# Kernel tuning notes

Hardware: AMD Instinct MI355X
Metric: run time of the kernel (lower is better)

Reference implementation:

```python
import jax, jax.numpy as jnp
import numpy as np

N = 20000       # nodes
E = 320000      # edges (before self-loops)
F_IN = 1024     # num_features
H = 4           # head_num
C = 64          # hidden_size
NC = 4          # n_classes
NEG_SLOPE = 0.2 # PyG GATConv default


def setup_inputs() -> dict:
    key = jax.random.key(0)
    ks = jax.random.split(key, 16)
    def w(k, shape, fan_in):
        return jax.random.normal(k, shape, dtype=jnp.float32) / np.sqrt(fan_in)
    x = jax.random.normal(ks[0], (N, F_IN), dtype=jnp.float32)
    edge_index = jax.random.randint(ks[1], (2, E), 0, N, dtype=jnp.int64)
    return {
        "x": x,
        "edge_index": edge_index,
        # layer 1: F_IN -> H*C, concat
        "w1": w(ks[2], (F_IN, H * C), F_IN),
        "as1": w(ks[3], (H, C), C),
        "ad1": w(ks[4], (H, C), C),
        "b1": jnp.zeros((H * C,), jnp.float32),
        # layer 2: H*C -> H*C, concat
        "w2": w(ks[5], (H * C, H * C), H * C),
        "as2": w(ks[6], (H, C), C),
        "ad2": w(ks[7], (H, C), C),
        "b2": jnp.zeros((H * C,), jnp.float32),
        # out layer: H*C -> C, 1 head, concat=False
        "w3": w(ks[8], (H * C, 1 * C), H * C),
        "as3": w(ks[9], (1, C), C),
        "ad3": w(ks[10], (1, C), C),
        "b3": jnp.zeros((C,), jnp.float32),
        # classifier
        "wc": w(ks[11], (C, NC), C),
        "bc": jnp.zeros((NC,), jnp.float32),
    }


def gat_layer(x, src, dst, W, a_src, a_dst, bias, concat):
    """PyG GATConv (eval mode, self-loops already added to src/dst)."""
    n = x.shape[0]
    Hh, Cc = a_src.shape
    h = (x @ W).reshape(n, Hh, Cc)                       # [N,H,C]
    al_s = jnp.sum(h * a_src[None], axis=-1)             # [N,H]
    al_d = jnp.sum(h * a_dst[None], axis=-1)             # [N,H]
    e = al_s[src] + al_d[dst]                            # [E,H]
    e = jax.nn.leaky_relu(e, NEG_SLOPE)
    # segment softmax over incoming edges of each destination node
    emax = jax.ops.segment_max(e, dst, num_segments=n)   # [N,H]
    ex = jnp.exp(e - emax[dst])
    denom = jax.ops.segment_sum(ex, dst, num_segments=n) # [N,H]
    alpha = ex / (denom[dst] + 1e-16)                    # [E,H]
    msg = h[src] * alpha[..., None]                      # [E,H,C]
    out = jax.ops.segment_sum(msg, dst, num_segments=n)  # [N,H,C]
    if concat:
        out = out.reshape(n, Hh * Cc)
    else:
        out = out.mean(axis=1)
    return out + bias


def reference(x, edge_index, w1, as1, ad1, b1, w2, as2, ad2, b2,
              w3, as3, ad3, b3, wc, bc):
    n = x.shape[0]
    loop = jnp.arange(n, dtype=edge_index.dtype)
    src = jnp.concatenate([edge_index[0], loop])
    dst = jnp.concatenate([edge_index[1], loop])
    out = jax.nn.relu(gat_layer(x, src, dst, w1, as1, ad1, b1, True))
    out = jax.nn.relu(gat_layer(out, src, dst, w2, as2, ad2, b2, True))
    out = gat_layer(out, src, dst, w3, as3, ad3, b3, False)
    return out @ wc + bc                                  # [N, n_classes]
```

## Files before the change

kernel.cpp:

```cpp
#include <hip/hip_runtime.h>

#define N_NODES 20000
#define N_EDGES 320000
#define ET (N_EDGES + N_NODES)
#define F_IN 1024
#define HC 256
#define NC 4

typedef unsigned short ushort_t;
typedef __attribute__((ext_vector_type(8))) short short8;
typedef __attribute__((ext_vector_type(4))) float f32x4;

__device__ inline ushort_t f2bf(float f) {
    unsigned u = __float_as_uint(f);
    unsigned r = (u + 0x7fffu + ((u >> 16) & 1u)) >> 16;
    return (ushort_t)r;
}
__device__ inline float bf2f(ushort_t u) {
    return __uint_as_float(((unsigned)u) << 16);
}

#define GLOAD16(gp, lp) __builtin_amdgcn_global_load_lds( \
    (const __attribute__((address_space(1))) void*)(gp),  \
    (__attribute__((address_space(3))) void*)(lp), 16, 0, 0)

__global__ void count_kernel(const int* __restrict__ ei, int* __restrict__ counts) {
    int e = blockIdx.x * blockDim.x + threadIdx.x;
    if (e >= ET) return;
    int dst = (e < N_EDGES) ? ei[N_EDGES + e] : (e - N_EDGES);
    atomicAdd(&counts[dst], 1);
}

__global__ void scan_kernel(const int* __restrict__ counts, int* __restrict__ row_ptr,
                            int* __restrict__ cursor) {
    __shared__ int sums[1024];
    int t = threadIdx.x;
    const int per = (N_NODES + 1023) / 1024;
    int b = t * per;
    int e = min(b + per, N_NODES);
    int s = 0;
    for (int i = b; i < e; ++i) s += counts[i];
    sums[t] = s;
    __syncthreads();
    for (int off = 1; off < 1024; off <<= 1) {
        int v = (t >= off) ? sums[t - off] : 0;
        __syncthreads();
        sums[t] += v;
        __syncthreads();
    }
    int run = (t == 0) ? 0 : sums[t - 1];
    for (int i = b; i < e; ++i) {
        row_ptr[i] = run;
        cursor[i]  = run;
        run += counts[i];
    }
    if (t == 0) row_ptr[N_NODES] = ET;
}

__global__ void scatter_kernel(const int* __restrict__ ei, int* __restrict__ cursor,
                               int* __restrict__ col) {
    int e = blockIdx.x * blockDim.x + threadIdx.x;
    if (e >= ET) return;
    int src, dst;
    if (e < N_EDGES) { src = ei[e]; dst = ei[N_EDGES + e]; }
    else             { src = dst = e - N_EDGES; }
    int pos = atomicAdd(&cursor[dst], 1);
    col[pos] = src;
}

__global__ void split_rows(const float* __restrict__ in, ushort_t* __restrict__ hi,
                           ushort_t* __restrict__ lo, int n4) {
    int i = blockIdx.x * blockDim.x + threadIdx.x;
    int stride = gridDim.x * blockDim.x;
    for (; i < n4; i += stride) {
        float4 v = ((const float4*)in)[i];
        ushort4 h, l;
        h.x = f2bf(v.x); l.x = f2bf(v.x - bf2f(h.x));
        h.y = f2bf(v.y); l.y = f2bf(v.y - bf2f(h.y));
        h.z = f2bf(v.z); l.z = f2bf(v.z - bf2f(h.z));
        h.w = f2bf(v.w); l.w = f2bf(v.w - bf2f(h.w));
        ((ushort4*)hi)[i] = h;
        ((ushort4*)lo)[i] = l;
    }
}

__global__ void split_T(const float* __restrict__ in, ushort_t* __restrict__ hi,
                        ushort_t* __restrict__ lo, int K, int Nn) {
    int idx = blockIdx.x * blockDim.x + threadIdx.x;
    if (idx >= K * Nn) return;
    int k = idx / Nn, n = idx - k * Nn;
    float v = in[idx];
    ushort_t h = f2bf(v);
    hi[(size_t)n * K + k] = h;
    lo[(size_t)n * K + k] = f2bf(v - bf2f(h));
}

template<int BM, int BN, int GY>
__launch_bounds__(256)
__global__ void gemm_mfma(const ushort_t* __restrict__ Ah, const ushort_t* __restrict__ Al,
                          const ushort_t* __restrict__ BTh, const ushort_t* __restrict__ BTl,
                          float* __restrict__ C, int M, int K, int NT) {
    constexpr int SM = BM / 2;
    constexpr int SN = BN / 2;
    constexpr int MF = SM / 16;
    constexpr int NF = SN / 16;
    constexpr int AQ = BM / 64;
    constexpr int BQ = BN / 64;
    __shared__ __align__(16) ushort_t smem[(2 * BM + 2 * BN) * 32];
    char* Ash = (char*)smem;
    char* Asl = Ash + BM * 64;
    char* Bsh = Asl + BM * 64;
    char* Bsl = Bsh + BN * 64;

    const int t = threadIdx.x, lane = t & 63, w = t >> 6;
    const int wm = w >> 1, wn = w & 1;
    const int nwg = gridDim.x;
    const int id = blockIdx.x;
    const int q = nwg >> 3, r = nwg & 7;
    const int xcd = id & 7, idx = id >> 3;
    const int logical = (xcd < r ? xcd * (q + 1) : r * (q + 1) + (xcd - r) * q) + idx;
    const int bm = (logical / GY) * BM, bn = (logical % GY) * BN;
    const int gchunk = ((lane & 3) ^ ((lane >> 3) & 3)) * 16;

    size_t gA[AQ]; int lA[AQ];
    #pragma unroll
    for (int qq = 0; qq < AQ; ++qq) {
        int inst = w * AQ + qq;
        int row  = inst * 16 + (lane >> 2);
        int grow = min(bm + row, M - 1);
        gA[qq] = (size_t)grow * K * 2 + gchunk;
        lA[qq] = inst * 1024;
    }
    size_t gB[BQ]; int lB[BQ];
    #pragma unroll
    for (int qq = 0; qq < BQ; ++qq) {
        int inst = w * BQ + qq;
        int row  = inst * 16 + (lane >> 2);
        gB[qq] = (size_t)(bn + row) * K * 2 + gchunk;
        lB[qq] = inst * 1024;
    }

    f32x4 acc[MF][NF];
    #pragma unroll
    for (int i = 0; i < MF; ++i)
        #pragma unroll
        for (int j = 0; j < NF; ++j) acc[i][j] = (f32x4){0.f, 0.f, 0.f, 0.f};

    const char* Ahb = (const char*)Ah;
    const char* Alb = (const char*)Al;
    const char* Bhb = (const char*)BTh;
    const char* Blb = (const char*)BTl;
    const int c16 = (lane >> 4);

    for (int k0 = 0; k0 < K; k0 += 32) {
        size_t kb = (size_t)k0 * 2;
        #pragma unroll
        for (int qq = 0; qq < AQ; ++qq) {
            GLOAD16(Ahb + gA[qq] + kb, Ash + lA[qq]);
            GLOAD16(Alb + gA[qq] + kb, Asl + lA[qq]);
        }
        #pragma unroll
        for (int qq = 0; qq < BQ; ++qq) {
            GLOAD16(Bhb + gB[qq] + kb, Bsh + lB[qq]);
            GLOAD16(Blb + gB[qq] + kb, Bsl + lB[qq]);
        }
        __syncthreads();
        short8 afh[MF], afl[MF], bfh[NF], bfl[NF];
        #pragma unroll
        for (int i = 0; i < MF; ++i) {
            int row = wm * SM + i * 16 + (lane & 15);
            int off = row * 64 + ((c16 ^ ((row >> 1) & 3)) * 16);
            afh[i] = *(const short8*)(Ash + off);
            afl[i] = *(const short8*)(Asl + off);
        }
        #pragma unroll
        for (int j = 0; j < NF; ++j) {
            int row = wn * SN + j * 16 + (lane & 15);
            int off = row * 64 + ((c16 ^ ((row >> 1) & 3)) * 16);
            bfh[j] = *(const short8*)(Bsh + off);
            bfl[j] = *(const short8*)(Bsl + off);
        }
        #pragma unroll
        for (int i = 0; i < MF; ++i)
            #pragma unroll
            for (int j = 0; j < NF; ++j) {
                acc[i][j] = __builtin_amdgcn_mfma_f32_16x16x32_bf16(afh[i], bfh[j], acc[i][j], 0, 0, 0);
                acc[i][j] = __builtin_amdgcn_mfma_f32_16x16x32_bf16(afh[i], bfl[j], acc[i][j], 0, 0, 0);
                acc[i][j] = __builtin_amdgcn_mfma_f32_16x16x32_bf16(afl[i], bfh[j], acc[i][j], 0, 0, 0);
            }
        __syncthreads();
    }
    #pragma unroll
    for (int i = 0; i < MF; ++i) {
        int rbase = bm + wm * SM + i * 16 + (lane >> 4) * 4;
        #pragma unroll
        for (int j = 0; j < NF; ++j) {
            int col = bn + wn * SN + j * 16 + (lane & 15);
            #pragma unroll
            for (int rr = 0; rr < 4; ++rr)
                if (rbase + rr < M) C[(size_t)(rbase + rr) * NT + col] = acc[i][j][rr];
        }
    }
}

template<int H>
__global__ void al_kernel(const float* __restrict__ h, const float* __restrict__ as_w,
                          const float* __restrict__ ad_w, float* __restrict__ als,
                          float* __restrict__ ald) {
    int n = blockIdx.x;
    int t = threadIdx.x;
    float hv = h[(size_t)n * (H * 64) + t];
    float s = hv * as_w[t];
    float d = hv * ad_w[t];
    #pragma unroll
    for (int off = 32; off > 0; off >>= 1) {
        s += __shfl_down(s, off, 64);
        d += __shfl_down(d, off, 64);
    }
    if ((t & 63) == 0) {
        int head = t >> 6;
        als[n * H + head] = s;
        ald[n * H + head] = d;
    }
}

template<bool SPLIT>
__launch_bounds__(256)
__global__ void agg4_kernel(const float* __restrict__ h, const float* __restrict__ als,
                            const float* __restrict__ ald, const int* __restrict__ row_ptr,
                            const int* __restrict__ col, const float* __restrict__ bias,
                            ushort_t* __restrict__ oh, ushort_t* __restrict__ ol,
                            float* __restrict__ of) {
    int dst = blockIdx.x;
    int t = threadIdx.x, lane = t & 63, w = t >> 6;
    int beg = row_ptr[dst], deg = row_ptr[dst + 1] - beg;
    __shared__ float s_redm[4][4], s_redd[4][4];
    __shared__ float s_m[4], s_rden[4];
    __shared__ int   s_src[64];
    __shared__ float s_alpha[64][4];
    __shared__ float4 s_part[3][64];

    int i_loc = t >> 2, hh = t & 3;
    float ad = ald[dst * 4 + hh];

    float m = -1e30f, den = 0.f;
    for (int base = 0; base < deg; base += 64) {
        int i = base + i_loc;
        if (i < deg) {
            int src = col[beg + i];
            float e = als[src * 4 + hh] + ad;
            e = (e > 0.f) ? e : 0.2f * e;
            float nm = fmaxf(m, e);
            den = den * __expf(m - nm) + __expf(e - nm);
            m = nm;
        }
    }
    #pragma unroll
    for (int off = 4; off < 64; off <<= 1) {
        float mo = __shfl_xor(m, off, 64);
        float dn = __shfl_xor(den, off, 64);
        float nm = fmaxf(m, mo);
        den = den * __expf(m - nm) + dn * __expf(mo - nm);
        m = nm;
    }
    if (lane < 4) { s_redm[w][lane] = m; s_redd[w][lane] = den; }
    __syncthreads();
    if (t < 4) {
        float M = -1e30f, D = 0.f;
        #pragma unroll
        for (int ww = 0; ww < 4; ++ww) {
            float mo = s_redm[ww][t], dn = s_redd[ww][t];
            float nm = fmaxf(M, mo);
            D = D * __expf(M - nm) + dn * __expf(mo - nm);
            M = nm;
        }
        s_m[t] = M;
        s_rden[t] = 1.f / (D + 1e-16f);
    }
    __syncthreads();

    float mh = s_m[hh], rdh = s_rden[hh];
    float4 acc = make_float4(0.f, 0.f, 0.f, 0.f);
    int c = lane;
    int ghead = c >> 4;
    for (int base = 0; base < deg; base += 64) {
        int cn = min(64, deg - base);
        if (i_loc < cn) {
            int src = col[beg + base + i_loc];
            if (hh == 0) s_src[i_loc] = src;
            float e = als[src * 4 + hh] + ad;
            e = (e > 0.f) ? e : 0.2f * e;
            s_alpha[i_loc][hh] = __expf(e - mh) * rdh;
        }
        __syncthreads();
        for (int e = w; e < cn; e += 4) {
            int src = s_src[e];
            float a = s_alpha[e][ghead];
            float4 hv = *(const float4*)&h[(size_t)src * HC + c * 4];
            acc.x += a * hv.x; acc.y += a * hv.y;
            acc.z += a * hv.z; acc.w += a * hv.w;
        }
        __syncthreads();
    }
    if (w > 0) s_part[w - 1][c] = acc;
    __syncthreads();
    if (w == 0) {
        float4 p1 = s_part[0][c], p2 = s_part[1][c], p3 = s_part[2][c];
        float4 bv = *(const float4*)&bias[c * 4];
        float v0 = fmaxf(((acc.x + p1.x) + p2.x) + p3.x + bv.x, 0.f);
        float v1 = fmaxf(((acc.y + p1.y) + p2.y) + p3.y + bv.y, 0.f);
        float v2 = fmaxf(((acc.z + p1.z) + p2.z) + p3.z + bv.z, 0.f);
        float v3 = fmaxf(((acc.w + p1.w) + p2.w) + p3.w + bv.w, 0.f);
        size_t idx = (size_t)dst * HC + c * 4;
        if (SPLIT) {
            ushort4 h4, l4;
            h4.x = f2bf(v0); l4.x = f2bf(v0 - bf2f(h4.x));
            h4.y = f2bf(v1); l4.y = f2bf(v1 - bf2f(h4.y));
            h4.z = f2bf(v2); l4.z = f2bf(v2 - bf2f(h4.z));
            h4.w = f2bf(v3); l4.w = f2bf(v3 - bf2f(h4.w));
            *(ushort4*)&oh[idx] = h4;
            *(ushort4*)&ol[idx] = l4;
        } else {
            *(float4*)&of[idx] = make_float4(v0, v1, v2, v3);
        }
    }
}

__launch_bounds__(256)
__global__ void agg1_kernel(const float* __restrict__ h, const float* __restrict__ als,
                            const float* __restrict__ ald, const int* __restrict__ row_ptr,
                            const int* __restrict__ col, const float* __restrict__ bias,
                            float* __restrict__ of) {
    __shared__ int   s1_src[4][64];
    __shared__ float s1_alpha[4][64];
    int lane = threadIdx.x & 63, w = threadIdx.x >> 6;
    int dst = blockIdx.x * 4 + w;
    if (dst >= N_NODES) return;
    int beg = row_ptr[dst], deg = row_ptr[dst + 1] - beg;
    float ad = ald[dst];

    float m = -1e30f, den = 0.f;
    for (int base = 0; base < deg; base += 64) {
        int i = base + lane;
        if (i < deg) {
            float e = als[col[beg + i]] + ad;
            e = (e > 0.f) ? e : 0.2f * e;
            float nm = fmaxf(m, e);
            den = den * __expf(m - nm) + __expf(e - nm);
            m = nm;
        }
    }
    #pragma unroll
    for (int off = 1; off < 64; off <<= 1) {
        float mo = __shfl_xor(m, off, 64);
        float dn = __shfl_xor(den, off, 64);
        float nm = fmaxf(m, mo);
        den = den * __expf(m - nm) + dn * __expf(mo - nm);
        m = nm;
    }
    float rden = 1.f / (den + 1e-16f);

    float4 acc = make_float4(0.f, 0.f, 0.f, 0.f);
    int c = lane & 15, team = lane >> 4;
    for (int base = 0; base < deg; base += 64) {
        int cn = min(64, deg - base);
        if (lane < cn) {
            int src = col[beg + base + lane];
            s1_src[w][lane] = src;
            float e = als[src] + ad;
            e = (e > 0.f) ? e : 0.2f * e;
            s1_alpha[w][lane] = __expf(e - m) * rden;
        }
        for (int e = team; e < cn; e += 4) {
            float a = s1_alpha[w][e];
            float4 hv = *(const float4*)&h[(size_t)s1_src[w][e] * 64 + c * 4];
            acc.x += a * hv.x; acc.y += a * hv.y;
            acc.z += a * hv.z; acc.w += a * hv.w;
        }
    }
    acc.x += __shfl_xor(acc.x, 16, 64);
    acc.y += __shfl_xor(acc.y, 16, 64);
    acc.z += __shfl_xor(acc.z, 16, 64);
    acc.w += __shfl_xor(acc.w, 16, 64);
    acc.x += __shfl_xor(acc.x, 32, 64);
    acc.y += __shfl_xor(acc.y, 32, 64);
    acc.z += __shfl_xor(acc.z, 32, 64);
    acc.w += __shfl_xor(acc.w, 32, 64);
    if (team == 0) {
        float4 bv = *(const float4*)&bias[c * 4];
        *(float4*)&of[(size_t)dst * 64 + c * 4] =
            make_float4(acc.x + bv.x, acc.y + bv.y, acc.z + bv.z, acc.w + bv.w);
    }
}

__global__ void classifier_kernel(const float* __restrict__ x, const float* __restrict__ wc,
                                  const float* __restrict__ bc, float* __restrict__ out) {
    int n = blockIdx.x * blockDim.x + threadIdx.x;
    if (n >= N_NODES) return;
    float acc[NC] = {bc[0], bc[1], bc[2], bc[3]};
    for (int c = 0; c < 64; ++c) {
        float xv = x[(size_t)n * 64 + c];
        #pragma unroll
        for (int k = 0; k < NC; ++k) acc[k] += xv * wc[c * NC + k];
    }
    #pragma unroll
    for (int k = 0; k < NC; ++k) out[(size_t)n * NC + k] = acc[k];
}

extern "C" void kernel_launch(void* const* d_in, const int* in_sizes, int n_in,
                              void* d_out, int out_size, void* d_ws, size_t ws_size,
                              hipStream_t stream) {
    const float* x   = (const float*)d_in[0];
    const int*   ei  = (const int*)d_in[1];
    const float* w1  = (const float*)d_in[2];
    const float* as1 = (const float*)d_in[3];
    const float* ad1 = (const float*)d_in[4];
    const float* b1  = (const float*)d_in[5];
    const float* w2  = (const float*)d_in[6];
    const float* as2 = (const float*)d_in[7];
    const float* ad2 = (const float*)d_in[8];
    const float* b2  = (const float*)d_in[9];
    const float* w3  = (const float*)d_in[10];
    const float* as3 = (const float*)d_in[11];
    const float* ad3 = (const float*)d_in[12];
    const float* b3  = (const float*)d_in[13];
    const float* wc  = (const float*)d_in[14];
    const float* bc  = (const float*)d_in[15];
    float* out = (float*)d_out;

    char* ws = (char*)d_ws;
    size_t off = 0;
    auto alloc = [&](size_t bytes) -> char* {
        char* p = ws + off;
        off = (off + bytes + 255) & ~(size_t)255;
        return p;
    };

    int* counts  = (int*)alloc(N_NODES * 4);
    int* cursor  = (int*)alloc(N_NODES * 4);
    int* row_ptr = (int*)alloc((N_NODES + 1) * 4);
    int* colidx  = (int*)alloc(ET * 4);
    float* als   = (float*)alloc(N_NODES * 4 * 4);
    float* ald   = (float*)alloc(N_NODES * 4 * 4);
    float* B0    = (float*)alloc((size_t)N_NODES * HC * 4);

    ushort_t* xh   = (ushort_t*)alloc((size_t)N_NODES * F_IN * 2);
    ushort_t* xl   = (ushort_t*)alloc((size_t)N_NODES * F_IN * 2);
    ushort_t* w1Th = (ushort_t*)alloc((size_t)F_IN * HC * 2);
    ushort_t* w1Tl = (ushort_t*)alloc((size_t)F_IN * HC * 2);
    ushort_t* w2Th = (ushort_t*)alloc((size_t)HC * HC * 2);
    ushort_t* w2Tl = (ushort_t*)alloc((size_t)HC * HC * 2);
    ushort_t* w3Th = (ushort_t*)alloc((size_t)HC * 64 * 2);
    ushort_t* w3Tl = (ushort_t*)alloc((size_t)HC * 64 * 2);
    ushort_t* B1h  = (ushort_t*)alloc((size_t)N_NODES * HC * 2);
    ushort_t* B1l  = (ushort_t*)alloc((size_t)N_NODES * HC * 2);
    float*    B1f  = (float*)alloc((size_t)N_NODES * 64 * 4);

    hipMemsetAsync(counts, 0, N_NODES * sizeof(int), stream);
    int eb = (ET + 255) / 256;
    count_kernel<<<eb, 256, 0, stream>>>(ei, counts);
    scan_kernel<<<1, 1024, 0, stream>>>(counts, row_ptr, cursor);
    scatter_kernel<<<eb, 256, 0, stream>>>(ei, cursor, colidx);

    split_rows<<<2048, 256, 0, stream>>>(x, xh, xl, (int)((size_t)N_NODES * F_IN / 4));
    split_T<<<(F_IN * HC + 255) / 256, 256, 0, stream>>>(w1, w1Th, w1Tl, F_IN, HC);
    split_T<<<(HC * HC + 255) / 256, 256, 0, stream>>>(w2, w2Th, w2Tl, HC, HC);
    split_T<<<(HC * 64 + 255) / 256, 256, 0, stream>>>(w3, w3Th, w3Tl, HC, 64);

    const int nwg12 = ((N_NODES + 127) / 128) * (HC / 64);
    gemm_mfma<128, 64, 4><<<nwg12, 256, 0, stream>>>(xh, xl, w1Th, w1Tl, B0, N_NODES, F_IN, HC);
    al_kernel<4><<<N_NODES, 256, 0, stream>>>(B0, as1, ad1, als, ald);
    agg4_kernel<true><<<N_NODES, 256, 0, stream>>>(B0, als, ald, row_ptr, colidx, b1, B1h, B1l, nullptr);
    gemm_mfma<128, 64, 4><<<nwg12, 256, 0, stream>>>(B1h, B1l, w2Th, w2Tl, B0, N_NODES, HC, HC);
    al_kernel<4><<<N_NODES, 256, 0, stream>>>(B0, as2, ad2, als, ald);
    agg4_kernel<true><<<N_NODES, 256, 0, stream>>>(B0, als, ald, row_ptr, colidx, b2, B1h, B1l, nullptr);
    const int nwg3 = (N_NODES + 63) / 64;
    gemm_mfma<64, 64, 1><<<nwg3, 256, 0, stream>>>(B1h, B1l, w3Th, w3Tl, B0, N_NODES, HC, 64);
    al_kernel<1><<<N_NODES, 64, 0, stream>>>(B0, as3, ad3, als, ald);
    agg1_kernel<<<(N_NODES + 3) / 4, 256, 0, stream>>>(B0, als, ald, row_ptr, colidx, b3, B1f);
    classifier_kernel<<<(N_NODES + 255) / 256, 256, 0, stream>>>(B1f, wc, bc, out);
}
```

Before: 336.4 us.

## Split GAT aggregation into alpha precompute and channel-sliced gather kernels

Splits each GAT aggregation into two kernels. A separate kernel computes the per-edge softmax coefficients, stored head-major in a workspace buffer. A channel-sliced gather kernel then launches one wave per destination node per 32-channel slice, with the block order interleaved so that workgroups sharing a slice run together and reuse the L2-resident slice of the feature matrix. This replaces the per-destination 256-thread blocks and their shared-memory syncs, and adds two-way unrolled accumulation. In exchange it writes and reads an extra alpha array and recomputes the row pointers and column reads once per slice.

```diff
diff --git a/kernel.cpp b/kernel.cpp
--- a/kernel.cpp
+++ b/kernel.cpp
@@ -224,31 +224,23 @@
     }
 }
 
-template<bool SPLIT>
+template<int H>
 __launch_bounds__(256)
-__global__ void agg4_kernel(const float* __restrict__ h, const float* __restrict__ als,
-                            const float* __restrict__ ald, const int* __restrict__ row_ptr,
-                            const int* __restrict__ col, const float* __restrict__ bias,
-                            ushort_t* __restrict__ oh, ushort_t* __restrict__ ol,
-                            float* __restrict__ of) {
-    int dst = blockIdx.x;
-    int t = threadIdx.x, lane = t & 63, w = t >> 6;
+__global__ void alpha_kernel(const float* __restrict__ als, const float* __restrict__ ald,
+                             const int* __restrict__ row_ptr, const int* __restrict__ col,
+                             float* __restrict__ alpha) {
+    int lane = threadIdx.x & 63, w = threadIdx.x >> 6;
+    int dst = blockIdx.x * 4 + w;
+    if (dst >= N_NODES) return;
     int beg = row_ptr[dst], deg = row_ptr[dst + 1] - beg;
-    __shared__ float s_redm[4][4], s_redd[4][4];
-    __shared__ float s_m[4], s_rden[4];
-    __shared__ int   s_src[64];
-    __shared__ float s_alpha[64][4];
-    __shared__ float4 s_part[3][64];
-
-    int i_loc = t >> 2, hh = t & 3;
-    float ad = ald[dst * 4 + hh];
-
+    constexpr int ES = 64 / H;
+    int i_loc = lane / H, hh = lane % H;
+    float ad = ald[dst * H + hh];
     float m = -1e30f, den = 0.f;
-    for (int base = 0; base < deg; base += 64) {
+    for (int base = 0; base < deg; base += ES) {
         int i = base + i_loc;
         if (i < deg) {
-            int src = col[beg + i];
-            float e = als[src * 4 + hh] + ad;
+            float e = als[col[beg + i] * H + hh] + ad;
             e = (e > 0.f) ? e : 0.2f * e;
             float nm = fmaxf(m, e);
             den = den * __expf(m - nm) + __expf(e - nm);
@@ -256,62 +248,79 @@
         }
     }
     #pragma unroll
-    for (int off = 4; off < 64; off <<= 1) {
+    for (int off = H; off < 64; off <<= 1) {
         float mo = __shfl_xor(m, off, 64);
         float dn = __shfl_xor(den, off, 64);
         float nm = fmaxf(m, mo);
         den = den * __expf(m - nm) + dn * __expf(mo - nm);
         m = nm;
     }
-    if (lane < 4) { s_redm[w][lane] = m; s_redd[w][lane] = den; }
-    __syncthreads();
-    if (t < 4) {
-        float M = -1e30f, D = 0.f;
-        #pragma unroll
-        for (int ww = 0; ww < 4; ++ww) {
-            float mo = s_redm[ww][t], dn = s_redd[ww][t];
-            float nm = fmaxf(M, mo);
-            D = D * __expf(M - nm) + dn * __expf(mo - nm);
-            M = nm;
-        }
-        s_m[t] = M;
-        s_rden[t] = 1.f / (D + 1e-16f);
-    }
-    __syncthreads();
-
-    float mh = s_m[hh], rdh = s_rden[hh];
-    float4 acc = make_float4(0.f, 0.f, 0.f, 0.f);
-    int c = lane;
-    int ghead = c >> 4;
-    for (int base = 0; base < deg; base += 64) {
-        int cn = min(64, deg - base);
-        if (i_loc < cn) {
-            int src = col[beg + base + i_loc];
-            if (hh == 0) s_src[i_loc] = src;
-            float e = als[src * 4 + hh] + ad;
+    float rden = 1.f / (den + 1e-16f);
+    for (int base = 0; base < deg; base += ES) {
+        int i = base + i_loc;
+        if (i < deg) {
+            float e = als[col[beg + i] * H + hh] + ad;
             e = (e > 0.f) ? e : 0.2f * e;
-            s_alpha[i_loc][hh] = __expf(e - mh) * rdh;
-        }
-        __syncthreads();
-        for (int e = w; e < cn; e += 4) {
-            int src = s_src[e];
-            float a = s_alpha[e][ghead];
-            float4 hv = *(const float4*)&h[(size_t)src * HC + c * 4];
-            acc.x += a * hv.x; acc.y += a * hv.y;
-            acc.z += a * hv.z; acc.w += a * hv.w;
-        }
-        __syncthreads();
-    }
-    if (w > 0) s_part[w - 1][c] = acc;
-    __syncthreads();
-    if (w == 0) {
-        float4 p1 = s_part[0][c], p2 = s_part[1][c], p3 = s_part[2][c];
-        float4 bv = *(const float4*)&bias[c * 4];
-        float v0 = fmaxf(((acc.x + p1.x) + p2.x) + p3.x + bv.x, 0.f);
-        float v1 = fmaxf(((acc.y + p1.y) + p2.y) + p3.y + bv.y, 0.f);
-        float v2 = fmaxf(((acc.z + p1.z) + p2.z) + p3.z + bv.z, 0.f);
-        float v3 = fmaxf(((acc.w + p1.w) + p2.w) + p3.w + bv.w, 0.f);
-        size_t idx = (size_t)dst * HC + c * 4;
+            alpha[(size_t)hh * ET + beg + i] = __expf(e - m) * rden;
+        }
+    }
+}
+
+template<int CT, int NS, int H, bool RELU, bool SPLIT>
+__launch_bounds__(256)
+__global__ void agg_sliced(const float* __restrict__ h, const float* __restrict__ alpha,
+                           const int* __restrict__ row_ptr, const int* __restrict__ col,
+                           const float* __restrict__ bias,
+                           ushort_t* __restrict__ oh, ushort_t* __restrict__ ol,
+                           float* __restrict__ of) {
+    constexpr int CW = CT / NS;
+    const int nwg = gridDim.x;
+    const int q = nwg >> 3;
+    int id = blockIdx.x;
+    int logical = (id & 7) * q + (id >> 3);
+    int slice = logical / (N_NODES / 4);
+    int g = logical % (N_NODES / 4);
+    int lane = threadIdx.x & 63, w = threadIdx.x >> 6;
+    int dst = g * 4 + w;
+    int c = lane & 7, team = lane >> 3;
+    int beg = row_ptr[dst], deg = row_ptr[dst + 1] - beg;
+    const float* alphaS = alpha + (size_t)(slice * H / NS) * ET;
+    const float* hS = h + slice * CW;
+
+    float4 acc  = make_float4(0.f, 0.f, 0.f, 0.f);
+    float4 acc2 = make_float4(0.f, 0.f, 0.f, 0.f);
+    int e = team;
+    for (; e + 8 < deg; e += 16) {
+        int   s0 = col[beg + e],        s1 = col[beg + e + 8];
+        float a0 = alphaS[beg + e],     a1 = alphaS[beg + e + 8];
+        float4 h0 = *(const float4*)&hS[(size_t)s0 * CT + c * 4];
+        float4 h1 = *(const float4*)&hS[(size_t)s1 * CT + c * 4];
+        acc.x  += a0 * h0.x; acc.y  += a0 * h0.y; acc.z  += a0 * h0.z; acc.w  += a0 * h0.w;
+        acc2.x += a1 * h1.x; acc2.y += a1 * h1.y; acc2.z += a1 * h1.z; acc2.w += a1 * h1.w;
+    }
+    if (e < deg) {
+        int   s0 = col[beg + e];
+        float a0 = alphaS[beg + e];
+        float4 h0 = *(const float4*)&hS[(size_t)s0 * CT + c * 4];
+        acc.x += a0 * h0.x; acc.y += a0 * h0.y; acc.z += a0 * h0.z; acc.w += a0 * h0.w;
+    }
+    acc.x += acc2.x; acc.y += acc2.y; acc.z += acc2.z; acc.w += acc2.w;
+    #pragma unroll
+    for (int off = 8; off < 64; off <<= 1) {
+        acc.x += __shfl_xor(acc.x, off, 64);
+        acc.y += __shfl_xor(acc.y, off, 64);
+        acc.z += __shfl_xor(acc.z, off, 64);
+        acc.w += __shfl_xor(acc.w, off, 64);
+    }
+    if (team == 0) {
+        int ch = slice * CW + c * 4;
+        float4 bv = *(const float4*)&bias[ch];
+        float v0 = acc.x + bv.x, v1 = acc.y + bv.y, v2 = acc.z + bv.z, v3 = acc.w + bv.w;
+        if (RELU) {
+            v0 = fmaxf(v0, 0.f); v1 = fmaxf(v1, 0.f);
+            v2 = fmaxf(v2, 0.f); v3 = fmaxf(v3, 0.f);
+        }
+        size_t idx = (size_t)dst * CT + ch;
         if (SPLIT) {
             ushort4 h4, l4;
             h4.x = f2bf(v0); l4.x = f2bf(v0 - bf2f(h4.x));
@@ -323,73 +332,6 @@
         } else {
             *(float4*)&of[idx] = make_float4(v0, v1, v2, v3);
         }
-    }
-}
-
-__launch_bounds__(256)
-__global__ void agg1_kernel(const float* __restrict__ h, const float* __restrict__ als,
-                            const float* __restrict__ ald, const int* __restrict__ row_ptr,
-                            const int* __restrict__ col, const float* __restrict__ bias,
-                            float* __restrict__ of) {
-    __shared__ int   s1_src[4][64];
-    __shared__ float s1_alpha[4][64];
-    int lane = threadIdx.x & 63, w = threadIdx.x >> 6;
-    int dst = blockIdx.x * 4 + w;
-    if (dst >= N_NODES) return;
-    int beg = row_ptr[dst], deg = row_ptr[dst + 1] - beg;
-    float ad = ald[dst];
-
-    float m = -1e30f, den = 0.f;
-    for (int base = 0; base < deg; base += 64) {
-        int i = base + lane;
-        if (i < deg) {
-            float e = als[col[beg + i]] + ad;
-            e = (e > 0.f) ? e : 0.2f * e;
-            float nm = fmaxf(m, e);
-            den = den * __expf(m - nm) + __expf(e - nm);
-            m = nm;
-        }
-    }
-    #pragma unroll
-    for (int off = 1; off < 64; off <<= 1) {
-        float mo = __shfl_xor(m, off, 64);
-        float dn = __shfl_xor(den, off, 64);
-        float nm = fmaxf(m, mo);
-        den = den * __expf(m - nm) + dn * __expf(mo - nm);
-        m = nm;
-    }
-    float rden = 1.f / (den + 1e-16f);
-
-    float4 acc = make_float4(0.f, 0.f, 0.f, 0.f);
-    int c = lane & 15, team = lane >> 4;
-    for (int base = 0; base < deg; base += 64) {
-        int cn = min(64, deg - base);
-        if (lane < cn) {
-            int src = col[beg + base + lane];
-            s1_src[w][lane] = src;
-            float e = als[src] + ad;
-            e = (e > 0.f) ? e : 0.2f * e;
-            s1_alpha[w][lane] = __expf(e - m) * rden;
-        }
-        for (int e = team; e < cn; e += 4) {
-            float a = s1_alpha[w][e];
-            float4 hv = *(const float4*)&h[(size_t)s1_src[w][e] * 64 + c * 4];
-            acc.x += a * hv.x; acc.y += a * hv.y;
-            acc.z += a * hv.z; acc.w += a * hv.w;
-        }
-    }
-    acc.x += __shfl_xor(acc.x, 16, 64);
-    acc.y += __shfl_xor(acc.y, 16, 64);
-    acc.z += __shfl_xor(acc.z, 16, 64);
-    acc.w += __shfl_xor(acc.w, 16, 64);
-    acc.x += __shfl_xor(acc.x, 32, 64);
-    acc.y += __shfl_xor(acc.y, 32, 64);
-    acc.z += __shfl_xor(acc.z, 32, 64);
-    acc.w += __shfl_xor(acc.w, 32, 64);
-    if (team == 0) {
-        float4 bv = *(const float4*)&bias[c * 4];
-        *(float4*)&of[(size_t)dst * 64 + c * 4] =
-            make_float4(acc.x + bv.x, acc.y + bv.y, acc.z + bv.z, acc.w + bv.w);
     }
 }
 
@@ -442,6 +384,7 @@
     int* colidx  = (int*)alloc(ET * 4);
     float* als   = (float*)alloc(N_NODES * 4 * 4);
     float* ald   = (float*)alloc(N_NODES * 4 * 4);
+    float* alpha = (float*)alloc((size_t)4 * ET * 4);
     float* B0    = (float*)alloc((size_t)N_NODES * HC * 4);
 
     ushort_t* xh   = (ushort_t*)alloc((size_t)N_NODES * F_IN * 2);
@@ -468,15 +411,22 @@
     split_T<<<(HC * 64 + 255) / 256, 256, 0, stream>>>(w3, w3Th, w3Tl, HC, 64);
 
     const int nwg12 = ((N_NODES + 127) / 128) * (HC / 64);
+    const int nblk_dst = N_NODES / 4;
     gemm_mfma<128, 64, 4><<<nwg12, 256, 0, stream>>>(xh, xl, w1Th, w1Tl, B0, N_NODES, F_IN, HC);
     al_kernel<4><<<N_NODES, 256, 0, stream>>>(B0, as1, ad1, als, ald);
-    agg4_kernel<true><<<N_NODES, 256, 0, stream>>>(B0, als, ald, row_ptr, colidx, b1, B1h, B1l, nullptr);
+    alpha_kernel<4><<<nblk_dst, 256, 0, stream>>>(als, ald, row_ptr, colidx, alpha);
+    agg_sliced<256, 8, 4, true, true><<<8 * nblk_dst, 256, 0, stream>>>(
+        B0, alpha, row_ptr, colidx, b1, B1h, B1l, nullptr);
     gemm_mfma<128, 64, 4><<<nwg12, 256, 0, stream>>>(B1h, B1l, w2Th, w2Tl, B0, N_NODES, HC, HC);
     al_kernel<4><<<N_NODES, 256, 0, stream>>>(B0, as2, ad2, als, ald);
-    agg4_kernel<true><<<N_NODES, 256, 0, stream>>>(B0, als, ald, row_ptr, colidx, b2, B1h, B1l, nullptr);
+    alpha_kernel<4><<<nblk_dst, 256, 0, stream>>>(als, ald, row_ptr, colidx, alpha);
+    agg_sliced<256, 8, 4, true, true><<<8 * nblk_dst, 256, 0, stream>>>(
+        B0, alpha, row_ptr, colidx, b2, B1h, B1l, nullptr);
     const int nwg3 = (N_NODES + 63) / 64;
     gemm_mfma<64, 64, 1><<<nwg3, 256, 0, stream>>>(B1h, B1l, w3Th, w3Tl, B0, N_NODES, HC, 64);
     al_kernel<1><<<N_NODES, 64, 0, stream>>>(B0, as3, ad3, als, ald);
-    agg1_kernel<<<(N_NODES + 3) / 4, 256, 0, stream>>>(B0, als, ald, row_ptr, colidx, b3, B1f);
+    alpha_kernel<1><<<nblk_dst, 256, 0, stream>>>(als, ald, row_ptr, colidx, alpha);
+    agg_sliced<64, 2, 1, false, false><<<2 * nblk_dst, 256, 0, stream>>>(
+        B0, alpha, row_ptr, colidx, b3, nullptr, nullptr, B1f);
     classifier_kernel<<<(N_NODES + 255) / 256, 256, 0, stream>>>(B1f, wc, bc, out);
 }
```

Measured after the change: 363.1 us. 1.08x slower.
